# Kernel tuning notes

Hardware: AMD Instinct MI355X
Metric: run time of the kernel (lower is better)

## Reference

```python
import jax, jax.numpy as jnp
import numpy as np

D = 128      # internal_dimensions
L = 4        # num_edge_convs
N = 100000   # nodes
E = 800000   # edges
G = 64       # graphs
IN = 4       # in_channels


def _ln(x, g, b):
    m = jnp.mean(x, -1, keepdims=True)
    v = jnp.mean((x - m) ** 2, -1, keepdims=True)
    return (x - m) * jax.lax.rsqrt(v + 1e-5) * g + b


def _gelu(x):
    return jax.nn.gelu(x, approximate=False)  # torch nn.GELU default (erf)


def _seg_mean(x, seg, n):
    s = jax.ops.segment_sum(x, seg, num_segments=n)
    c = jax.ops.segment_sum(jnp.ones((x.shape[0], 1), x.dtype), seg, num_segments=n)
    return s / jnp.maximum(c, 1.0)


def _seg_max(x, seg, n):
    m = jax.ops.segment_max(x, seg, num_segments=n)
    return jnp.where(jnp.isfinite(m), m, 0.0)  # empty segments -> 0 (PyG convention)


def _forward(x, edge_index, batch, num_graphs,
             in_W1, in_b1, in_g1, in_bn1, in_W2, in_b2, in_g2, in_bn2,
             pre_g, pre_b, cW1, cb1, cg1, cbb1, cW2, cb2, cg2, cbb2, pW, pb,
             ag_g, ag_b,
             kW1, kb1, kg1, kbb1, kW2, kb2, kg2, kbb2,
             kW3, kb3, kg3, kbb3, kW4, kb4):
    n = x.shape[0]
    # input_net: Linear -> LN -> GELU -> Linear -> LN   (dropout=0, eval)
    h = _gelu(_ln(x @ in_W1 + in_b1, in_g1, in_bn1))
    h = _ln(h @ in_W2 + in_b2, in_g2, in_bn2)

    x_in_max = _seg_max(h, batch, num_graphs)
    x_in_mean = _seg_mean(h, batch, num_graphs)

    src, dst = edge_index[0], edge_index[1]  # PyG: message from src (x_j) to dst (x_i)
    xcur = h
    for l in range(L):
        identity = xcur
        hn = _ln(xcur, pre_g[l], pre_b[l])
        xi = hn[dst]            # [E, D]
        xj = hn[src]            # [E, D]
        m = jnp.concatenate([xi, xj - xi], axis=-1)       # [E, 2D]
        m = _gelu(_ln(m @ cW1[l] + cb1[l], cg1[l], cbb1[l]))
        m = _gelu(_ln(m @ cW2[l] + cb2[l], cg2[l], cbb2[l]))
        a_max = _seg_max(m, dst, n)
        a_mean = _seg_mean(m, dst, n)
        aggr = jnp.concatenate([a_max, a_mean], axis=-1)  # [N, 2D]
        xcur = identity + aggr @ pW[l] + pb[l]

    xcur = _ln(xcur, ag_g, ag_b)
    x_g_max = _seg_max(xcur, batch, num_graphs)
    x_g_mean = _seg_mean(xcur, batch, num_graphs)

    xp = jnp.concatenate([x_in_max, x_in_mean, x_g_max, x_g_mean], axis=-1)  # [G, 4D]
    z = _gelu(_ln(xp @ kW1 + kb1, kg1, kbb1))
    z = _gelu(_ln(z @ kW2 + kb2, kg2, kbb2))
    z = _gelu(_ln(z @ kW3 + kb3, kg3, kbb3))
    return z @ kW4 + kb4  # [G, 1]


def setup_inputs() -> dict:
    key = jax.random.key(0)
    ks = iter(jax.random.split(key, 64))
    def W(shape, fan):
        return jax.random.normal(next(ks), shape, jnp.float32) * np.float32((2.0 / fan) ** 0.5)
    inp = {}
    inp["x"] = jax.random.normal(next(ks), (N, IN), jnp.float32)
    inp["edge_index"] = jax.random.randint(next(ks), (2, E), 0, N)
    inp["batch"] = jnp.sort(jax.random.randint(next(ks), (N,), 0, G))
    inp["num_graphs"] = G
    inp["in_W1"] = W((IN, D), IN); inp["in_b1"] = jnp.zeros((D,), jnp.float32)
    inp["in_g1"] = jnp.ones((D,), jnp.float32); inp["in_bn1"] = jnp.zeros((D,), jnp.float32)
    inp["in_W2"] = W((D, D), D); inp["in_b2"] = jnp.zeros((D,), jnp.float32)
    inp["in_g2"] = jnp.ones((D,), jnp.float32); inp["in_bn2"] = jnp.zeros((D,), jnp.float32)
    inp["pre_g"] = jnp.ones((L, D), jnp.float32); inp["pre_b"] = jnp.zeros((L, D), jnp.float32)
    inp["cW1"] = W((L, 2 * D, D), 2 * D); inp["cb1"] = jnp.zeros((L, D), jnp.float32)
    inp["cg1"] = jnp.ones((L, D), jnp.float32); inp["cbb1"] = jnp.zeros((L, D), jnp.float32)
    inp["cW2"] = W((L, D, D), D); inp["cb2"] = jnp.zeros((L, D), jnp.float32)
    inp["cg2"] = jnp.ones((L, D), jnp.float32); inp["cbb2"] = jnp.zeros((L, D), jnp.float32)
    inp["pW"] = W((L, 2 * D, D), 2 * D); inp["pb"] = jnp.zeros((L, D), jnp.float32)
    inp["ag_g"] = jnp.ones((D,), jnp.float32); inp["ag_b"] = jnp.zeros((D,), jnp.float32)
    inp["kW1"] = W((4 * D, D), 4 * D); inp["kb1"] = jnp.zeros((D,), jnp.float32)
    inp["kg1"] = jnp.ones((D,), jnp.float32); inp["kbb1"] = jnp.zeros((D,), jnp.float32)
    inp["kW2"] = W((D, D), D); inp["kb2"] = jnp.zeros((D,), jnp.float32)
    inp["kg2"] = jnp.ones((D,), jnp.float32); inp["kbb2"] = jnp.zeros((D,), jnp.float32)
    inp["kW3"] = W((D, D // 4), D); inp["kb3"] = jnp.zeros((D // 4,), jnp.float32)
    inp["kg3"] = jnp.ones((D // 4,), jnp.float32); inp["kbb3"] = jnp.zeros((D // 4,), jnp.float32)
    inp["kW4"] = W((D // 4, 1), D // 4); inp["kb4"] = jnp.zeros((1,), jnp.float32)
    return inp


def reference(x, edge_index, batch, num_graphs,
              in_W1, in_b1, in_g1, in_bn1, in_W2, in_b2, in_g2, in_bn2,
              pre_g, pre_b, cW1, cb1, cg1, cbb1, cW2, cb2, cg2, cbb2, pW, pb,
              ag_g, ag_b,
              kW1, kb1, kg1, kbb1, kW2, kb2, kg2, kbb2,
              kW3, kb3, kg3, kbb3, kW4, kb4):
    return _forward(x, edge_index, batch, num_graphs,
                    in_W1, in_b1, in_g1, in_bn1, in_W2, in_b2, in_g2, in_bn2,
                    pre_g, pre_b, cW1, cb1, cg1, cbb1, cW2, cb2, cg2, cbb2, pW, pb,
                    ag_g, ag_b,
                    kW1, kb1, kg1, kbb1, kW2, kb2, kg2, kbb2,
                    kW3, kb3, kg3, kbb3, kW4, kb4)
```

## Files before the change

kernel.cpp:

```cpp
#include <hip/hip_runtime.h>
#include <hip/hip_bf16.h>
#include <math.h>

__device__ __forceinline__ float geluf(float x) {
    return 0.5f * x * (1.0f + erff(x * 0.70710678118654752f));
}
#define MAPNEGINF 0x007FFFFFu
__device__ __forceinline__ float funmap(unsigned m) {
    return __uint_as_float((m & 0x80000000u) ? (m ^ 0x80000000u) : ~m);
}
__device__ __forceinline__ unsigned fmap(float f) {
    unsigned u = __float_as_uint(f);
    return ((int)u < 0) ? ~u : (u | 0x80000000u);
}
__device__ __forceinline__ float wred64(float v) {
#pragma unroll
    for (int m = 1; m < 64; m <<= 1) v += __shfl_xor(v, m);
    return v;
}
__device__ __forceinline__ unsigned short bf16r(float f) {
    unsigned u = __float_as_uint(f);
    u += 0x7fffu + ((u >> 16) & 1u);
    return (unsigned short)(u >> 16);
}

__device__ __forceinline__ void stage_wq(float* Ws, const float* __restrict__ src, int t) {
#pragma unroll
    for (int it = 0; it < 4; ++it) {
        const int idx = it * 1024 + (t << 2);
        *(float4*)(Ws + idx) = *(const float4*)(src + idx);
    }
}

__device__ __forceinline__ void kloop_q(const float* As, const float* Ws, float (&acc)[4][8],
                                        const int r0, const int ogc, const int kb) {
#pragma unroll
    for (int kk = 0; kk < 32; kk += 4) {
        const float4 a0 = *(const float4*)(As + (r0 + 0) * 132 + kb + kk);
        const float4 a1 = *(const float4*)(As + (r0 + 1) * 132 + kb + kk);
        const float4 a2 = *(const float4*)(As + (r0 + 2) * 132 + kb + kk);
        const float4 a3 = *(const float4*)(As + (r0 + 3) * 132 + kb + kk);
#define MAD8(R, AV)                                                                     \
    {                                                                                   \
        acc[R][0] += (AV)*wA.x; acc[R][1] += (AV)*wA.y; acc[R][2] += (AV)*wA.z;         \
        acc[R][3] += (AV)*wA.w; acc[R][4] += (AV)*wB.x; acc[R][5] += (AV)*wB.y;         \
        acc[R][6] += (AV)*wB.z; acc[R][7] += (AV)*wB.w;                                 \
    }
#define KSTEP(J, C)                                                                     \
    {                                                                                   \
        const float4 wA = *(const float4*)(Ws + (kk + (J)) * 128 + ogc);                \
        const float4 wB = *(const float4*)(Ws + (kk + (J)) * 128 + 64 + ogc);           \
        MAD8(0, a0.C) MAD8(1, a1.C) MAD8(2, a2.C) MAD8(3, a3.C)                         \
    }
        KSTEP(0, x) KSTEP(1, y) KSTEP(2, z) KSTEP(3, w)
#undef KSTEP
#undef MAD8
    }
}

__global__ void k_zero(unsigned* __restrict__ p, int n) {
    const int i = blockIdx.x * 256 + threadIdx.x;
    if (i < n) p[i] = 0u;
}

__global__ void k_copyu(const unsigned* __restrict__ a, const unsigned* __restrict__ b,
                        unsigned* __restrict__ ac, unsigned* __restrict__ bc, int n) {
    const int i = blockIdx.x * 256 + threadIdx.x;
    if (i < n) {
        ac[i] = a[i];
        bc[i] = b[i];
    }
}

__global__ void k_count(const int* __restrict__ ei, unsigned* __restrict__ deg, int E) {
    const int e = blockIdx.x * 256 + threadIdx.x;
    if (e < E) atomicAdd(deg + ei[E + e], 1u);
}

__global__ void k_scan1(const unsigned* __restrict__ deg, unsigned* __restrict__ excl,
                        unsigned* __restrict__ bsum, int n) {
    __shared__ unsigned sh[256];
    const int t = threadIdx.x;
    const int base = blockIdx.x * 1024 + t * 4;
    unsigned v0 = (base + 0 < n) ? deg[base + 0] : 0u;
    unsigned v1 = (base + 1 < n) ? deg[base + 1] : 0u;
    unsigned v2 = (base + 2 < n) ? deg[base + 2] : 0u;
    unsigned v3 = (base + 3 < n) ? deg[base + 3] : 0u;
    const unsigned s = v0 + v1 + v2 + v3;
    sh[t] = s;
    __syncthreads();
    for (int off = 1; off < 256; off <<= 1) {
        unsigned x = 0;
        if (t >= off) x = sh[t - off];
        __syncthreads();
        if (t >= off) sh[t] += x;
        __syncthreads();
    }
    const unsigned ebase = sh[t] - s;
    if (base + 0 < n) excl[base + 0] = ebase;
    if (base + 1 < n) excl[base + 1] = ebase + v0;
    if (base + 2 < n) excl[base + 2] = ebase + v0 + v1;
    if (base + 3 < n) excl[base + 3] = ebase + v0 + v1 + v2;
    if (t == 255) bsum[blockIdx.x] = sh[255];
}

__global__ void k_scan2(unsigned* __restrict__ bsum, int nb) {
    __shared__ unsigned sh[256];
    const int t = threadIdx.x;
    const unsigned v = (t < nb) ? bsum[t] : 0u;
    sh[t] = v;
    __syncthreads();
    for (int off = 1; off < 256; off <<= 1) {
        unsigned x = 0;
        if (t >= off) x = sh[t - off];
        __syncthreads();
        if (t >= off) sh[t] += x;
        __syncthreads();
    }
    if (t < nb) bsum[t] = sh[t] - v;
}

__global__ void k_scan3(unsigned* __restrict__ excl, const unsigned* __restrict__ bsum, int n) {
    const int t = threadIdx.x;
    const int base = blockIdx.x * 1024 + t * 4;
    const unsigned add = bsum[blockIdx.x];
#pragma unroll
    for (int j = 0; j < 4; ++j)
        if (base + j < n) excl[base + j] += add;
}

__global__ void k_scatter(const int* __restrict__ ei, unsigned* __restrict__ cursor,
                          int* __restrict__ esrc, int* __restrict__ edst, int E) {
    const int e = blockIdx.x * 256 + threadIdx.x;
    if (e < E) {
        const int s = ei[e];
        const int d = ei[E + e];
        const unsigned pos = atomicAdd(cursor + d, 1u);
        esrc[pos] = s;
        edst[pos] = d;
    }
}

__global__ void k_in1(const float* __restrict__ x, const float* __restrict__ W1,
                      const float* __restrict__ b1, const float* __restrict__ g1,
                      const float* __restrict__ bn1, float* __restrict__ h, int n) {
    const int t = threadIdx.x, lane = t & 63, wave = t >> 6;
    const int d0 = lane << 1;
    const float2 w0 = *(const float2*)(W1 + d0);
    const float2 w1 = *(const float2*)(W1 + 128 + d0);
    const float2 w2 = *(const float2*)(W1 + 256 + d0);
    const float2 w3 = *(const float2*)(W1 + 384 + d0);
    const float2 bb = *(const float2*)(b1 + d0);
    const float2 gg = *(const float2*)(g1 + d0);
    const float2 nn = *(const float2*)(bn1 + d0);
    const int stride = gridDim.x * 4;
    for (int node = blockIdx.x * 4 + wave; node < n; node += stride) {
        const float4 xv = *(const float4*)(x + (size_t)node * 4);
        float h0 = bb.x + xv.x * w0.x + xv.y * w1.x + xv.z * w2.x + xv.w * w3.x;
        float h1 = bb.y + xv.x * w0.y + xv.y * w1.y + xv.z * w2.y + xv.w * w3.y;
        const float s = wred64(h0 + h1), q = wred64(h0 * h0 + h1 * h1);
        const float mean = s * 0.0078125f, var = q * 0.0078125f - mean * mean;
        const float rs = rsqrtf(var + 1e-5f);
        h0 = geluf((h0 - mean) * rs * gg.x + nn.x);
        h1 = geluf((h1 - mean) * rs * gg.y + nn.y);
        *(float2*)(h + (size_t)node * 128 + d0) = make_float2(h0, h1);
    }
}

__global__ __launch_bounds__(256, 2) void k_in2(const float* __restrict__ A,
                                                const float* __restrict__ W,
                                                const float* __restrict__ bias,
                                                const float* __restrict__ g,
                                                const float* __restrict__ b,
                                                float* __restrict__ C, int n) {
    __shared__ float As[64 * 132];
    __shared__ float Ws[4096];
    const int t = threadIdx.x;
    const int n0 = blockIdx.x * 64;
    {
        const int r = t >> 2, c0 = (t & 3) << 5;
        const int row = n0 + r;
        const bool ok = row < n;
#pragma unroll
        for (int j = 0; j < 8; ++j) {
            const int col = c0 + (j << 2);
            float4 v = make_float4(0.f, 0.f, 0.f, 0.f);
            if (ok) v = *(const float4*)(A + (size_t)row * 128 + col);
            *(float4*)(As + r * 132 + col) = v;
        }
    }
    float acc[4][8];
#pragma unroll
    for (int r = 0; r < 4; ++r)
#pragma unroll
        for (int o = 0; o < 8; ++o) acc[r][o] = 0.f;
    const int og = t & 15, eg = t >> 4;
    const int ogc = og << 2, r0 = eg << 2;
#pragma unroll
    for (int q4 = 0; q4 < 4; ++q4) {
        stage_wq(Ws, W + q4 * 4096, t);
        __syncthreads();
        kloop_q(As, Ws, acc, r0, ogc, q4 * 32);
        __syncthreads();
    }
    const float4 bA = *(const float4*)(bias + ogc);
    const float4 bB = *(const float4*)(bias + 64 + ogc);
    const float4 gA = *(const float4*)(g + ogc);
    const float4 gB = *(const float4*)(g + 64 + ogc);
    const float4 lA = *(const float4*)(b + ogc);
    const float4 lB = *(const float4*)(b + 64 + ogc);
#pragma unroll
    for (int r = 0; r < 4; ++r) {
        float v[8];
        v[0] = acc[r][0] + bA.x; v[1] = acc[r][1] + bA.y;
        v[2] = acc[r][2] + bA.z; v[3] = acc[r][3] + bA.w;
        v[4] = acc[r][4] + bB.x; v[5] = acc[r][5] + bB.y;
        v[6] = acc[r][6] + bB.z; v[7] = acc[r][7] + bB.w;
        float s = 0.f, q = 0.f;
#pragma unroll
        for (int o = 0; o < 8; ++o) { s += v[o]; q += v[o] * v[o]; }
#pragma unroll
        for (int m = 1; m < 16; m <<= 1) { s += __shfl_xor(s, m); q += __shfl_xor(q, m); }
        const float mean = s * 0.0078125f;
        const float var = q * 0.0078125f - mean * mean;
        const float rs = rsqrtf(var + 1e-5f);
        const int row = n0 + r0 + r;
        if (row < n) {
            *(float4*)(C + (size_t)row * 128 + ogc) = make_float4(
                (v[0] - mean) * rs * gA.x + lA.x, (v[1] - mean) * rs * gA.y + lA.y,
                (v[2] - mean) * rs * gA.z + lA.z, (v[3] - mean) * rs * gA.w + lA.w);
            *(float4*)(C + (size_t)row * 128 + 64 + ogc) = make_float4(
                (v[4] - mean) * rs * gB.x + lB.x, (v[5] - mean) * rs * gB.y + lB.y,
                (v[6] - mean) * rs * gB.z + lB.z, (v[7] - mean) * rs * gB.w + lB.w);
        }
    }
}

__global__ void k_ln(const float* __restrict__ in, const float* __restrict__ g,
                     const float* __restrict__ b, float* __restrict__ out, int n) {
    const int t = threadIdx.x, lane = t & 63, wave = t >> 6;
    const int d0 = lane << 1;
    const float ga = g[d0], gb = g[d0 + 1], ba = b[d0], bb = b[d0 + 1];
    const int stride = gridDim.x * 4;
    for (int node = blockIdx.x * 4 + wave; node < n; node += stride) {
        const float2 v = *(const float2*)(in + (size_t)node * 128 + d0);
        const float s = wred64(v.x + v.y), q = wred64(v.x * v.x + v.y * v.y);
        const float mean = s * 0.0078125f, var = q * 0.0078125f - mean * mean;
        const float rs = rsqrtf(var + 1e-5f);
        *(float2*)(out + (size_t)node * 128 + d0) =
            make_float2((v.x - mean) * rs * ga + ba, (v.y - mean) * rs * gb + bb);
    }
}

__global__ void k_wxj(const float* __restrict__ c, float* __restrict__ Wx,
                      float* __restrict__ Wj) {
    const int idx = blockIdx.x * 256 + threadIdx.x;
    const float a = c[idx], b = c[16384 + idx];
    Wx[idx] = a - b;
    Wj[idx] = b;
}

__global__ __launch_bounds__(256, 2) void k_gemmh(const float* __restrict__ A,
                                                  const float* __restrict__ W,
                                                  const float* __restrict__ bias,
                                                  unsigned short* __restrict__ C, int n) {
    __shared__ float As[64 * 132];
    __shared__ float Ws[4096];
    const int t = threadIdx.x;
    const int n0 = blockIdx.x * 64;
    {
        const int r = t >> 2, c0 = (t & 3) << 5;
        const int row = n0 + r;
        const bool ok = row < n;
#pragma unroll
        for (int j = 0; j < 8; ++j) {
            const int col = c0 + (j << 2);
            float4 v = make_float4(0.f, 0.f, 0.f, 0.f);
            if (ok) v = *(const float4*)(A + (size_t)row * 128 + col);
            *(float4*)(As + r * 132 + col) = v;
        }
    }
    float acc[4][8];
#pragma unroll
    for (int r = 0; r < 4; ++r)
#pragma unroll
        for (int o = 0; o < 8; ++o) acc[r][o] = 0.f;
    const int og = t & 15, eg = t >> 4;
    const int ogc = og << 2, r0 = eg << 2;
#pragma unroll
    for (int q4 = 0; q4 < 4; ++q4) {
        stage_wq(Ws, W + q4 * 4096, t);
        __syncthreads();
        kloop_q(As, Ws, acc, r0, ogc, q4 * 32);
        __syncthreads();
    }
    float4 bA = make_float4(0.f, 0.f, 0.f, 0.f), bB = bA;
    if (bias) {
        bA = *(const float4*)(bias + ogc);
        bB = *(const float4*)(bias + 64 + ogc);
    }
#pragma unroll
    for (int r = 0; r < 4; ++r) {
        const int row = n0 + r0 + r;
        if (row < n) {
            ushort4 u0, u1;
            u0.x = bf16r(acc[r][0] + bA.x); u0.y = bf16r(acc[r][1] + bA.y);
            u0.z = bf16r(acc[r][2] + bA.z); u0.w = bf16r(acc[r][3] + bA.w);
            u1.x = bf16r(acc[r][4] + bB.x); u1.y = bf16r(acc[r][5] + bB.y);
            u1.z = bf16r(acc[r][6] + bB.z); u1.w = bf16r(acc[r][7] + bB.w);
            *(ushort4*)(C + (size_t)row * 128 + ogc) = u0;
            *(ushort4*)(C + (size_t)row * 128 + 64 + ogc) = u1;
        }
    }
}

__global__ __launch_bounds__(256, 2) void k_edge(
    const unsigned short* __restrict__ P, const unsigned short* __restrict__ Q,
    const int* __restrict__ esrc, const int* __restrict__ edst, const float* __restrict__ W2,
    const float* __restrict__ g1, const float* __restrict__ b1, const float* __restrict__ cb2,
    const float* __restrict__ g2, const float* __restrict__ b2,
    const unsigned* __restrict__ rowend, const unsigned* __restrict__ degc,
    float* __restrict__ amax, float* __restrict__ asum, float* __restrict__ recmax,
    float* __restrict__ recsum, int* __restrict__ recid, int E) {
    __shared__ float Us[64 * 132];
    __shared__ float Ws[4096];
    __shared__ int sdst[64], ssrc[64], sdg[64];
    __shared__ float scb2[128], sg2[128], sb2[128];
    const int t = threadIdx.x;
    const int base = blockIdx.x * 512;
    if (t >= 128) {
        const int d = t - 128;
        scb2[d] = cb2[d];
        sg2[d] = g2[d];
        sb2[d] = b2[d];
    }
    const int lane = t & 63, wave = t >> 6;
    const int d0 = lane << 1;
    const float g1a = g1[d0], g1b = g1[d0 + 1], b1a = b1[d0], b1b = b1[d0 + 1];
    const int og = t & 15, eg = t >> 4;
    const int ogc = og << 2, r0 = eg << 2;
    int cur = -1, istart = 0;
    float vmax = -INFINITY, vsum = 0.f;
    int id0 = -1, id1 = -1;

    for (int s8 = 0; s8 < 8; ++s8) {
        const int sb = base + s8 * 64;
        __syncthreads();
        if (t < 64) {
            const int idx = sb + t;
            const int ci = idx < E ? idx : (E - 1);
            ssrc[t] = esrc[ci];
            const int d = edst[ci];
            sdg[t] = d;
            sdst[t] = (idx < E) ? d : -1;
        }
        __syncthreads();
#pragma unroll 4
        for (int p = 0; p < 16; ++p) {
            const int i = (p << 2) + wave;
            const unsigned pu = *(const unsigned*)(P + ((size_t)sdg[i] << 7) + d0);
            const unsigned qu = *(const unsigned*)(Q + ((size_t)ssrc[i] << 7) + d0);
            const float x0 = __uint_as_float(pu << 16) + __uint_as_float(qu << 16);
            const float x1 =
                __uint_as_float(pu & 0xffff0000u) + __uint_as_float(qu & 0xffff0000u);
            const float s = wred64(x0 + x1);
            const float q = wred64(x0 * x0 + x1 * x1);
            const float mean = s * 0.0078125f;
            const float var = q * 0.0078125f - mean * mean;
            const float rs = rsqrtf(var + 1e-5f);
            const float y0 = geluf((x0 - mean) * rs * g1a + b1a);
            const float y1 = geluf((x1 - mean) * rs * g1b + b1b);
            *(float2*)(Us + i * 132 + d0) = make_float2(y0, y1);
        }
        float acc[4][8];
#pragma unroll
        for (int r = 0; r < 4; ++r)
#pragma unroll
            for (int o = 0; o < 8; ++o) acc[r][o] = 0.f;
#pragma unroll
        for (int q4 = 0; q4 < 4; ++q4) {
            stage_wq(Ws, W2 + q4 * 4096, t);
            __syncthreads();
            kloop_q(Us, Ws, acc, r0, ogc, q4 * 32);
            __syncthreads();
        }
#pragma unroll
        for (int r = 0; r < 4; ++r) {
            float v[8];
            float s = 0.f, q = 0.f;
#pragma unroll
            for (int o = 0; o < 8; ++o) {
                const int col = (o < 4) ? (ogc + o) : (64 + ogc + o - 4);
                v[o] = acc[r][o] + scb2[col];
                s += v[o];
                q += v[o] * v[o];
            }
#pragma unroll
            for (int m = 1; m < 16; m <<= 1) { s += __shfl_xor(s, m); q += __shfl_xor(q, m); }
            const float mean = s * 0.0078125f;
            const float var = q * 0.0078125f - mean * mean;
            const float rs = rsqrtf(var + 1e-5f);
#pragma unroll
            for (int o = 0; o < 8; ++o) {
                const int col = (o < 4) ? (ogc + o) : (64 + ogc + o - 4);
                v[o] = geluf((v[o] - mean) * rs * sg2[col] + sb2[col]);
            }
            *(float4*)(Us + (r0 + r) * 132 + ogc) = make_float4(v[0], v[1], v[2], v[3]);
            *(float4*)(Us + (r0 + r) * 132 + 64 + ogc) = make_float4(v[4], v[5], v[6], v[7]);
        }
        __syncthreads();
        if (t < 128) {
            for (int i = 0; i < 64; ++i) {
                const int dn = sdst[i];
                const int gi = s8 * 64 + i;
                if (dn != cur) {
                    if (cur >= 0) {
                        const unsigned re = rowend[cur];
                        const unsigned rs0 = re - degc[cur];
                        const unsigned ps = (unsigned)(base + istart);
                        const unsigned pe = (unsigned)(base + gi);
                        if (ps == rs0 && pe == re) {
                            amax[(size_t)cur * 128 + t] = vmax;
                            asum[(size_t)cur * 128 + t] = vsum;
                        } else {
                            const int slot = (istart == 0) ? 0 : 1;
                            const size_t ro = (size_t)(2 * blockIdx.x + slot) * 128 + t;
                            recmax[ro] = vmax;
                            recsum[ro] = vsum;
                            if (slot == 0) id0 = cur; else id1 = cur;
                        }
                    }
                    cur = dn;
                    istart = gi;
                    vmax = -INFINITY;
                    vsum = 0.f;
                }
                if (dn >= 0) {
                    const float v = Us[i * 132 + t];
                    vmax = fmaxf(vmax, v);
                    vsum += v;
                }
            }
        }
    }
    if (t < 128 && cur >= 0) {
        const int iend = min(512, E - base);
        const unsigned re = rowend[cur];
        const unsigned rs0 = re - degc[cur];
        const unsigned ps = (unsigned)(base + istart);
        const unsigned pe = (unsigned)(base + iend);
        if (ps == rs0 && pe == re) {
            amax[(size_t)cur * 128 + t] = vmax;
            asum[(size_t)cur * 128 + t] = vsum;
        } else {
            const int slot = (istart == 0) ? 0 : 1;
            const size_t ro = (size_t)(2 * blockIdx.x + slot) * 128 + t;
            recmax[ro] = vmax;
            recsum[ro] = vsum;
            if (slot == 0) id0 = cur; else id1 = cur;
        }
    }
    if (t == 0) {
        recid[2 * blockIdx.x] = id0;
        recid[2 * blockIdx.x + 1] = id1;
    }
}

__global__ void k_merge(const unsigned* __restrict__ rowend, const unsigned* __restrict__ degc,
                        const float* __restrict__ recmax, const float* __restrict__ recsum,
                        const int* __restrict__ recid, float* __restrict__ amax,
                        float* __restrict__ asum, int n) {
    const int node = blockIdx.x * 2 + (threadIdx.x >> 7);
    const int t = threadIdx.x & 127;
    if (node >= n) return;
    const unsigned dg = degc[node];
    if (dg == 0u) {
        amax[(size_t)node * 128 + t] = 0.f;
        asum[(size_t)node * 128 + t] = 0.f;
        return;
    }
    const unsigned re = rowend[node], rs = re - dg;
    const int b0 = rs >> 9, b1 = (re - 1) >> 9;
    if (b0 == b1) return;
    float m = -INFINITY, s = 0.f;
    for (int b = b0; b <= b1; ++b) {
#pragma unroll
        for (int sl = 0; sl < 2; ++sl) {
            if (recid[2 * b + sl] == node) {
                const size_t ro = (size_t)(2 * b + sl) * 128 + t;
                m = fmaxf(m, recmax[ro]);
                s += recsum[ro];
            }
        }
    }
    amax[(size_t)node * 128 + t] = m;
    asum[(size_t)node * 128 + t] = s;
}

__global__ __launch_bounds__(256, 2) void k_update(const float* __restrict__ amax,
                                                   const float* __restrict__ asum,
                                                   const unsigned* __restrict__ degc,
                                                   const float* __restrict__ pW,
                                                   const float* __restrict__ pb,
                                                   float* __restrict__ xcur, int n) {
    __shared__ float As[64 * 132];
    __shared__ float Ws[4096];
    const int t = threadIdx.x;
    const int n0 = blockIdx.x * 64;
    const int og = t & 15, eg = t >> 4;
    const int ogc = og << 2, r0 = eg << 2;
    float acc[4][8];
#pragma unroll
    for (int r = 0; r < 4; ++r)
#pragma unroll
        for (int o = 0; o < 8; ++o) acc[r][o] = 0.f;
    const int r = t >> 2, c0 = (t & 3) << 5;
    const int row = n0 + r;
    const bool ok = row < n;
#pragma unroll
    for (int pass = 0; pass < 2; ++pass) {
        if (pass == 0) {
#pragma unroll
            for (int j = 0; j < 8; ++j) {
                const int col = c0 + (j << 2);
                float4 v = make_float4(0.f, 0.f, 0.f, 0.f);
                if (ok) v = *(const float4*)(amax + (size_t)row * 128 + col);
                *(float4*)(As + r * 132 + col) = v;
            }
        } else {
            float inv = 0.f;
            if (ok) {
                const unsigned dv = degc[row];
                inv = 1.f / (float)(dv < 1u ? 1u : dv);
            }
#pragma unroll
            for (int j = 0; j < 8; ++j) {
                const int col = c0 + (j << 2);
                float4 v = make_float4(0.f, 0.f, 0.f, 0.f);
                if (ok) {
                    const float4 sv = *(const float4*)(asum + (size_t)row * 128 + col);
                    v = make_float4(sv.x * inv, sv.y * inv, sv.z * inv, sv.w * inv);
                }
                *(float4*)(As + r * 132 + col) = v;
            }
        }
#pragma unroll
        for (int q4 = 0; q4 < 4; ++q4) {
            stage_wq(Ws, pW + (size_t)(pass * 128 + q4 * 32) * 128, t);
            __syncthreads();
            kloop_q(As, Ws, acc, r0, ogc, q4 * 32);
            __syncthreads();
        }
    }
    const float4 bA = *(const float4*)(pb + ogc);
    const float4 bB = *(const float4*)(pb + 64 + ogc);
#pragma unroll
    for (int rr = 0; rr < 4; ++rr) {
        const int orow = n0 + r0 + rr;
        if (orow < n) {
            const float4 x0 = *(const float4*)(xcur + (size_t)orow * 128 + ogc);
            const float4 x1 = *(const float4*)(xcur + (size_t)orow * 128 + 64 + ogc);
            *(float4*)(xcur + (size_t)orow * 128 + ogc) =
                make_float4(x0.x + acc[rr][0] + bA.x, x0.y + acc[rr][1] + bA.y,
                            x0.z + acc[rr][2] + bA.z, x0.w + acc[rr][3] + bA.w);
            *(float4*)(xcur + (size_t)orow * 128 + 64 + ogc) =
                make_float4(x1.x + acc[rr][4] + bB.x, x1.y + acc[rr][5] + bB.y,
                            x1.z + acc[rr][6] + bB.z, x1.w + acc[rr][7] + bB.w);
        }
    }
}

__global__ void k_pool_init(unsigned* __restrict__ gmax1, float* __restrict__ gsum1,
                            unsigned* __restrict__ gcount1, unsigned* __restrict__ gmax2,
                            float* __restrict__ gsum2, unsigned* __restrict__ gcount2, int ng) {
    const int i = blockIdx.x * 256 + threadIdx.x;
    if (i < ng * 128) {
        gmax1[i] = MAPNEGINF;
        gsum1[i] = 0.f;
        gmax2[i] = MAPNEGINF;
        gsum2[i] = 0.f;
    }
    if (i < ng) {
        gcount1[i] = 0u;
        gcount2[i] = 0u;
    }
}

__global__ void k_pool(const float* __restrict__ in, const int* __restrict__ batch,
                       unsigned* __restrict__ gmax, float* __restrict__ gsum,
                       unsigned* __restrict__ gcount, int n) {
    const int t = threadIdx.x;
    if (t >= 128) return;
    const int per = (n + gridDim.x - 1) / gridDim.x;
    const int i0 = blockIdx.x * per;
    const int i1 = min(n, i0 + per);
    if (i0 >= i1) return;
    int cur = batch[i0];
    float vmax = -INFINITY, vsum = 0.f;
    unsigned cnt = 0;
    for (int i = i0; i < i1; ++i) {
        const int g = batch[i];
        if (g != cur) {
            atomicMax(gmax + (size_t)cur * 128 + t, fmap(vmax));
            atomicAdd(gsum + (size_t)cur * 128 + t, vsum);
            if (t == 0) atomicAdd(gcount + cur, cnt);
            cur = g;
            vmax = -INFINITY;
            vsum = 0.f;
            cnt = 0;
        }
        const float v = in[(size_t)i * 128 + t];
        vmax = fmaxf(vmax, v);
        vsum += v;
        cnt++;
    }
    atomicMax(gmax + (size_t)cur * 128 + t, fmap(vmax));
    atomicAdd(gsum + (size_t)cur * 128 + t, vsum);
    if (t == 0) atomicAdd(gcount + cur, cnt);
}

__global__ void k_xp(const unsigned* __restrict__ gmax1, const float* __restrict__ gsum1,
                     const unsigned* __restrict__ gcount1, const unsigned* __restrict__ gmax2,
                     const float* __restrict__ gsum2, const unsigned* __restrict__ gcount2,
                     float* __restrict__ xp) {
    const int g = blockIdx.x, d = threadIdx.x;
    const unsigned c1u = gcount1[g], c2u = gcount2[g];
    const float c1 = (float)(c1u < 1u ? 1u : c1u);
    const float c2 = (float)(c2u < 1u ? 1u : c2u);
    const unsigned m1 = gmax1[g * 128 + d], m2 = gmax2[g * 128 + d];
    xp[g * 512 + d] = (m1 == MAPNEGINF) ? 0.f : funmap(m1);
    xp[g * 512 + 128 + d] = gsum1[g * 128 + d] / c1;
    xp[g * 512 + 256 + d] = (m2 == MAPNEGINF) ? 0.f : funmap(m2);
    xp[g * 512 + 384 + d] = gsum2[g * 128 + d] / c2;
}

__global__ __launch_bounds__(64) void k_know(
    const float* __restrict__ xp, const float* __restrict__ kW1, const float* __restrict__ kb1,
    const float* __restrict__ kg1, const float* __restrict__ kbb1, const float* __restrict__ kW2,
    const float* __restrict__ kb2, const float* __restrict__ kg2, const float* __restrict__ kbb2,
    const float* __restrict__ kW3, const float* __restrict__ kb3, const float* __restrict__ kg3,
    const float* __restrict__ kbb3, const float* __restrict__ kW4, const float* __restrict__ kb4,
    float* __restrict__ out) {
    __shared__ float sh[512];
    __shared__ float s3[32];
    const int l = threadIdx.x, g = blockIdx.x;
    const int d0 = l << 1;
    *(float4*)(sh + l * 8) = *(const float4*)(xp + g * 512 + l * 8);
    *(float4*)(sh + l * 8 + 4) = *(const float4*)(xp + g * 512 + l * 8 + 4);
    __syncthreads();
    float a0 = kb1[d0], a1 = kb1[d0 + 1];
    for (int k = 0; k < 512; ++k) {
        const float u = sh[k];
        const float2 w = *(const float2*)(kW1 + k * 128 + d0);
        a0 += u * w.x;
        a1 += u * w.y;
    }
    {
        const float s = wred64(a0 + a1), q = wred64(a0 * a0 + a1 * a1);
        const float mean = s * 0.0078125f, var = q * 0.0078125f - mean * mean;
        const float rs = rsqrtf(var + 1e-5f);
        a0 = geluf((a0 - mean) * rs * kg1[d0] + kbb1[d0]);
        a1 = geluf((a1 - mean) * rs * kg1[d0 + 1] + kbb1[d0 + 1]);
    }
    __syncthreads();
    sh[d0] = a0;
    sh[d0 + 1] = a1;
    __syncthreads();
    float b0v = kb2[d0], b1v = kb2[d0 + 1];
    for (int k = 0; k < 128; ++k) {
        const float u = sh[k];
        const float2 w = *(const float2*)(kW2 + k * 128 + d0);
        b0v += u * w.x;
        b1v += u * w.y;
    }
    {
        const float s = wred64(b0v + b1v), q = wred64(b0v * b0v + b1v * b1v);
        const float mean = s * 0.0078125f, var = q * 0.0078125f - mean * mean;
        const float rs = rsqrtf(var + 1e-5f);
        b0v = geluf((b0v - mean) * rs * kg2[d0] + kbb2[d0]);
        b1v = geluf((b1v - mean) * rs * kg2[d0 + 1] + kbb2[d0 + 1]);
    }
    __syncthreads();
    sh[d0] = b0v;
    sh[d0 + 1] = b1v;
    __syncthreads();
    const int d3 = (l & 15) << 1;
    float c0 = kb3[d3], c1 = kb3[d3 + 1];
    for (int k = 0; k < 128; ++k) {
        const float u = sh[k];
        const float2 w = *(const float2*)(kW3 + k * 32 + d3);
        c0 += u * w.x;
        c1 += u * w.y;
    }
    {
        float s = c0 + c1, q = c0 * c0 + c1 * c1;
#pragma unroll
        for (int m = 1; m < 16; m <<= 1) {
            s += __shfl_xor(s, m);
            q += __shfl_xor(q, m);
        }
        const float mean = s * 0.03125f, var = q * 0.03125f - mean * mean;
        const float rs = rsqrtf(var + 1e-5f);
        c0 = geluf((c0 - mean) * rs * kg3[d3] + kbb3[d3]);
        c1 = geluf((c1 - mean) * rs * kg3[d3 + 1] + kbb3[d3 + 1]);
    }
    if (l < 16) {
        s3[d3] = c0;
        s3[d3 + 1] = c1;
    }
    __syncthreads();
    if (l == 0) {
        float rr = kb4[0];
        for (int k = 0; k < 32; ++k) rr += s3[k] * kW4[k];
        out[g] = rr;
    }
}

extern "C" void kernel_launch(void* const* d_in, const int* in_sizes, int n_in, void* d_out,
                              int out_size, void* d_ws, size_t ws_size, hipStream_t stream) {
    const int N = in_sizes[0] / 4;
    const int E = in_sizes[1] / 2;
    const int G = 64;
    const int L = 4;

    const float* x = (const float*)d_in[0];
    const int* ei = (const int*)d_in[1];
    const int* batch = (const int*)d_in[2];
    const float* inW1 = (const float*)d_in[4];
    const float* inb1 = (const float*)d_in[5];
    const float* ing1 = (const float*)d_in[6];
    const float* inbn1 = (const float*)d_in[7];
    const float* inW2 = (const float*)d_in[8];
    const float* inb2 = (const float*)d_in[9];
    const float* ing2 = (const float*)d_in[10];
    const float* inbn2 = (const float*)d_in[11];
    const float* pre_g = (const float*)d_in[12];
    const float* pre_b = (const float*)d_in[13];
    const float* cW1 = (const float*)d_in[14];
    const float* cb1 = (const float*)d_in[15];
    const float* cg1 = (const float*)d_in[16];
    const float* cbb1 = (const float*)d_in[17];
    const float* cW2 = (const float*)d_in[18];
    const float* cb2 = (const float*)d_in[19];
    const float* cg2 = (const float*)d_in[20];
    const float* cbb2 = (const float*)d_in[21];
    const float* pW = (const float*)d_in[22];
    const float* pb = (const float*)d_in[23];
    const float* ag_g = (const float*)d_in[24];
    const float* ag_b = (const float*)d_in[25];
    const float* kW1 = (const float*)d_in[26];
    const float* kb1 = (const float*)d_in[27];
    const float* kg1 = (const float*)d_in[28];
    const float* kbb1 = (const float*)d_in[29];
    const float* kW2 = (const float*)d_in[30];
    const float* kb2 = (const float*)d_in[31];
    const float* kg2 = (const float*)d_in[32];
    const float* kbb2 = (const float*)d_in[33];
    const float* kW3 = (const float*)d_in[34];
    const float* kb3 = (const float*)d_in[35];
    const float* kg3 = (const float*)d_in[36];
    const float* kbb3 = (const float*)d_in[37];
    const float* kW4 = (const float*)d_in[38];
    const float* kb4 = (const float*)d_in[39];
    float* out = (float*)d_out;

    const int nblkE = (E + 511) / 512;

    char* wsb = (char*)d_ws;
    size_t off = 0;
    auto ALC = [&](size_t bytes) {
        void* p = wsb + off;
        off = (off + bytes + 255) & ~(size_t)255;
        return p;
    };
    const size_t NB = (size_t)N * 128 * 4;
    float* xcur = (float*)ALC(NB);
    float* hn = (float*)ALC(NB);
    float* amax = hn;
    float* asum = (float*)ALC(NB);
    unsigned short* Pb = (unsigned short*)ALC((size_t)N * 128 * 2);
    unsigned short* Qb = (unsigned short*)ALC((size_t)N * 128 * 2);
    unsigned* deg = (unsigned*)ALC((size_t)N * 4);
    unsigned* cursor = (unsigned*)ALC((size_t)N * 4);
    unsigned* degc = (unsigned*)ALC((size_t)N * 4);
    unsigned* rowend = (unsigned*)ALC((size_t)N * 4);
    unsigned* bsum = (unsigned*)ALC(4096);
    int* esrc = (int*)ALC((size_t)E * 4);
    int* edst = (int*)ALC((size_t)E * 4);
    float* recmax = (float*)ALC((size_t)nblkE * 2 * 128 * 4);
    float* recsum = (float*)ALC((size_t)nblkE * 2 * 128 * 4);
    int* recid = (int*)ALC((size_t)nblkE * 2 * 4);
    float* Wx = (float*)ALC(65536);
    float* Wj = (float*)ALC(65536);
    unsigned* gmax1 = (unsigned*)ALC((size_t)G * 128 * 4);
    float* gsum1 = (float*)ALC((size_t)G * 128 * 4);
    unsigned* gcount1 = (unsigned*)ALC((size_t)G * 4);
    unsigned* gmax2 = (unsigned*)ALC((size_t)G * 128 * 4);
    float* gsum2 = (float*)ALC((size_t)G * 128 * 4);
    unsigned* gcount2 = (unsigned*)ALC((size_t)G * 4);
    float* xp = (float*)ALC((size_t)G * 512 * 4);

    if (off > ws_size) {
        k_zero<<<(out_size + 255) / 256, 256, 0, stream>>>((unsigned*)d_out, out_size);
        return;
    }

    k_zero<<<(N + 255) / 256, 256, 0, stream>>>(deg, N);
    k_count<<<(E + 255) / 256, 256, 0, stream>>>(ei, deg, E);
    const int nb = (N + 1023) / 1024;
    k_scan1<<<nb, 256, 0, stream>>>(deg, cursor, bsum, N);
    k_scan2<<<1, 256, 0, stream>>>(bsum, nb);
    k_scan3<<<nb, 256, 0, stream>>>(cursor, bsum, N);
    k_scatter<<<(E + 255) / 256, 256, 0, stream>>>(ei, cursor, esrc, edst, E);
    k_copyu<<<(N + 255) / 256, 256, 0, stream>>>(deg, cursor, degc, rowend, N);

    const int gemmGrid = (N + 63) / 64;
    k_in1<<<1024, 256, 0, stream>>>(x, inW1, inb1, ing1, inbn1, hn, N);
    k_in2<<<gemmGrid, 256, 0, stream>>>(hn, inW2, inb2, ing2, inbn2, xcur, N);
    k_pool_init<<<(G * 128 + 255) / 256, 256, 0, stream>>>(gmax1, gsum1, gcount1, gmax2, gsum2,
                                                           gcount2, G);
    k_pool<<<512, 256, 0, stream>>>(xcur, batch, gmax1, gsum1, gcount1, N);

    for (int l = 0; l < L; ++l) {
        k_wxj<<<64, 256, 0, stream>>>(cW1 + (size_t)l * 32768, Wx, Wj);
        k_ln<<<1024, 256, 0, stream>>>(xcur, pre_g + l * 128, pre_b + l * 128, hn, N);
        k_gemmh<<<gemmGrid, 256, 0, stream>>>(hn, Wx, cb1 + l * 128, Pb, N);
        k_gemmh<<<gemmGrid, 256, 0, stream>>>(hn, Wj, (const float*)nullptr, Qb, N);
        k_edge<<<nblkE, 256, 0, stream>>>(Pb, Qb, esrc, edst, cW2 + (size_t)l * 16384,
                                          cg1 + l * 128, cbb1 + l * 128, cb2 + l * 128,
                                          cg2 + l * 128, cbb2 + l * 128, rowend, degc, amax, asum,
                                          recmax, recsum, recid, E);
        k_merge<<<(N + 1) / 2, 256, 0, stream>>>(rowend, degc, recmax, recsum, recid, amax, asum,
                                                 N);
        k_update<<<gemmGrid, 256, 0, stream>>>(amax, asum, degc, pW + (size_t)l * 32768,
                                               pb + l * 128, xcur, N);
    }

    k_ln<<<1024, 256, 0, stream>>>(xcur, ag_g, ag_b, hn, N);
    k_pool<<<512, 256, 0, stream>>>(hn, batch, gmax2, gsum2, gcount2, N);
    k_xp<<<G, 128, 0, stream>>>(gmax1, gsum1, gcount1, gmax2, gsum2, gcount2, xp);
    k_know<<<G, 64, 0, stream>>>(xp, kW1, kb1, kg1, kbb1, kW2, kb2, kg2, kbb2, kW3, kb3, kg3,
                                 kbb3, kW4, kb4, out);
}
```

Measured before the change: 95.78 ms.

## Split edge kernel into chunked gather pass and per-64-edge GEMM pass

The fused edge kernel (gather + LN/GELU + GEMM + segmented aggregation over 512 edges per block) is split into two kernels. A grid-stride gather kernel writes the normalized first-layer activations to an fp32 chunk buffer, and a GEMM kernel handles 64 edges per block with the segment reduction. Edges are processed in chunks so the buffer can stay cache-resident, and the merge and record granularity moves from 512 to 64 edges. The mean division also moves into a separate k_mean kernel. In exchange the activations make an extra round trip through memory, and there are more launches, more partial records to merge, and more weight restaging per block.

```diff
diff --git a/kernel.cpp b/kernel.cpp
--- a/kernel.cpp
+++ b/kernel.cpp
@@ -314,155 +314,144 @@
     }
 }
 
-__global__ __launch_bounds__(256, 2) void k_edge(
-    const unsigned short* __restrict__ P, const unsigned short* __restrict__ Q,
-    const int* __restrict__ esrc, const int* __restrict__ edst, const float* __restrict__ W2,
-    const float* __restrict__ g1, const float* __restrict__ b1, const float* __restrict__ cb2,
-    const float* __restrict__ g2, const float* __restrict__ b2,
+__global__ void k_gather(const unsigned short* __restrict__ P,
+                         const unsigned short* __restrict__ Q, const int* __restrict__ esrc,
+                         const int* __restrict__ edst, const float* __restrict__ g1,
+                         const float* __restrict__ b1, float* __restrict__ U, int e0, int e1) {
+    const int t = threadIdx.x, lane = t & 63, wave = t >> 6;
+    const int d0 = lane << 1;
+    const float ga = g1[d0], gb = g1[d0 + 1], ba = b1[d0], bb = b1[d0 + 1];
+    const int stride = gridDim.x * 4;
+    for (int e = e0 + blockIdx.x * 4 + wave; e < e1; e += stride) {
+        const int s = esrc[e], d = edst[e];
+        const unsigned pu = *(const unsigned*)(P + ((size_t)d << 7) + d0);
+        const unsigned qu = *(const unsigned*)(Q + ((size_t)s << 7) + d0);
+        const float x0 = __uint_as_float(pu << 16) + __uint_as_float(qu << 16);
+        const float x1 = __uint_as_float(pu & 0xffff0000u) + __uint_as_float(qu & 0xffff0000u);
+        const float su = wred64(x0 + x1);
+        const float qq = wred64(x0 * x0 + x1 * x1);
+        const float mean = su * 0.0078125f;
+        const float var = qq * 0.0078125f - mean * mean;
+        const float rs = rsqrtf(var + 1e-5f);
+        *(float2*)(U + (size_t)(e - e0) * 128 + d0) = make_float2(
+            geluf((x0 - mean) * rs * ga + ba), geluf((x1 - mean) * rs * gb + bb));
+    }
+}
+
+__global__ __launch_bounds__(256, 2) void k_gemme(
+    const float* __restrict__ U, const int* __restrict__ edst, const float* __restrict__ W2,
+    const float* __restrict__ cb2, const float* __restrict__ g2, const float* __restrict__ b2,
     const unsigned* __restrict__ rowend, const unsigned* __restrict__ degc,
     float* __restrict__ amax, float* __restrict__ asum, float* __restrict__ recmax,
-    float* __restrict__ recsum, int* __restrict__ recid, int E) {
+    float* __restrict__ recsum, int* __restrict__ recid, int e0, int E) {
     __shared__ float Us[64 * 132];
     __shared__ float Ws[4096];
-    __shared__ int sdst[64], ssrc[64], sdg[64];
+    __shared__ int sdst[64];
     __shared__ float scb2[128], sg2[128], sb2[128];
     const int t = threadIdx.x;
-    const int base = blockIdx.x * 512;
+    const int base = e0 + blockIdx.x * 64;
+    if (base >= E) return;
+    const int gb = base >> 6;
+    if (t < 64) {
+        const int idx = base + t;
+        sdst[t] = (idx < E) ? edst[idx] : -1;
+    }
     if (t >= 128) {
         const int d = t - 128;
         scb2[d] = cb2[d];
         sg2[d] = g2[d];
         sb2[d] = b2[d];
     }
-    const int lane = t & 63, wave = t >> 6;
-    const int d0 = lane << 1;
-    const float g1a = g1[d0], g1b = g1[d0 + 1], b1a = b1[d0], b1b = b1[d0 + 1];
+    {
+        const int r = t >> 2, c0 = (t & 3) << 5;
+        const bool ok = (base + r) < E;
+        const float* src = U + (size_t)(base - e0 + r) * 128;
+#pragma unroll
+        for (int j = 0; j < 8; ++j) {
+            const int col = c0 + (j << 2);
+            float4 v = make_float4(0.f, 0.f, 0.f, 0.f);
+            if (ok) v = *(const float4*)(src + col);
+            *(float4*)(Us + r * 132 + col) = v;
+        }
+    }
+    float acc[4][8];
+#pragma unroll
+    for (int r = 0; r < 4; ++r)
+#pragma unroll
+        for (int o = 0; o < 8; ++o) acc[r][o] = 0.f;
     const int og = t & 15, eg = t >> 4;
     const int ogc = og << 2, r0 = eg << 2;
-    int cur = -1, istart = 0;
-    float vmax = -INFINITY, vsum = 0.f;
-    int id0 = -1, id1 = -1;
-
-    for (int s8 = 0; s8 < 8; ++s8) {
-        const int sb = base + s8 * 64;
-        __syncthreads();
-        if (t < 64) {
-            const int idx = sb + t;
-            const int ci = idx < E ? idx : (E - 1);
-            ssrc[t] = esrc[ci];
-            const int d = edst[ci];
-            sdg[t] = d;
-            sdst[t] = (idx < E) ? d : -1;
-        }
-        __syncthreads();
-#pragma unroll 4
-        for (int p = 0; p < 16; ++p) {
-            const int i = (p << 2) + wave;
-            const unsigned pu = *(const unsigned*)(P + ((size_t)sdg[i] << 7) + d0);
-            const unsigned qu = *(const unsigned*)(Q + ((size_t)ssrc[i] << 7) + d0);
-            const float x0 = __uint_as_float(pu << 16) + __uint_as_float(qu << 16);
-            const float x1 =
-                __uint_as_float(pu & 0xffff0000u) + __uint_as_float(qu & 0xffff0000u);
-            const float s = wred64(x0 + x1);
-            const float q = wred64(x0 * x0 + x1 * x1);
-            const float mean = s * 0.0078125f;
-            const float var = q * 0.0078125f - mean * mean;
-            const float rs = rsqrtf(var + 1e-5f);
-            const float y0 = geluf((x0 - mean) * rs * g1a + b1a);
-            const float y1 = geluf((x1 - mean) * rs * g1b + b1b);
-            *(float2*)(Us + i * 132 + d0) = make_float2(y0, y1);
-        }
-        float acc[4][8];
-#pragma unroll
-        for (int r = 0; r < 4; ++r)
-#pragma unroll
-            for (int o = 0; o < 8; ++o) acc[r][o] = 0.f;
-#pragma unroll
-        for (int q4 = 0; q4 < 4; ++q4) {
-            stage_wq(Ws, W2 + q4 * 4096, t);
-            __syncthreads();
-            kloop_q(Us, Ws, acc, r0, ogc, q4 * 32);
-            __syncthreads();
-        }
-#pragma unroll
-        for (int r = 0; r < 4; ++r) {
-            float v[8];
-            float s = 0.f, q = 0.f;
-#pragma unroll
-            for (int o = 0; o < 8; ++o) {
-                const int col = (o < 4) ? (ogc + o) : (64 + ogc + o - 4);
-                v[o] = acc[r][o] + scb2[col];
-                s += v[o];
-                q += v[o] * v[o];
+#pragma unroll
+    for (int q4 = 0; q4 < 4; ++q4) {
+        stage_wq(Ws, W2 + q4 * 4096, t);
+        __syncthreads();
+        kloop_q(Us, Ws, acc, r0, ogc, q4 * 32);
+        __syncthreads();
+    }
+#pragma unroll
+    for (int r = 0; r < 4; ++r) {
+        float v[8];
+        float s = 0.f, q = 0.f;
+#pragma unroll
+        for (int o = 0; o < 8; ++o) {
+            const int col = (o < 4) ? (ogc + o) : (64 + ogc + o - 4);
+            v[o] = acc[r][o] + scb2[col];
+            s += v[o];
+            q += v[o] * v[o];
+        }
+#pragma unroll
+        for (int m = 1; m < 16; m <<= 1) { s += __shfl_xor(s, m); q += __shfl_xor(q, m); }
+        const float mean = s * 0.0078125f;
+        const float var = q * 0.0078125f - mean * mean;
+        const float rs = rsqrtf(var + 1e-5f);
+#pragma unroll
+        for (int o = 0; o < 8; ++o) {
+            const int col = (o < 4) ? (ogc + o) : (64 + ogc + o - 4);
+            v[o] = geluf((v[o] - mean) * rs * sg2[col] + sb2[col]);
+        }
+        *(float4*)(Us + (r0 + r) * 132 + ogc) = make_float4(v[0], v[1], v[2], v[3]);
+        *(float4*)(Us + (r0 + r) * 132 + 64 + ogc) = make_float4(v[4], v[5], v[6], v[7]);
+    }
+    __syncthreads();
+    if (t < 128) {
+        int cur = sdst[0], istart = 0;
+        float vmax = -INFINITY, vsum = 0.f;
+        int id0 = -1, id1 = -1;
+        auto flush = [&](int iend) {
+            const unsigned re = rowend[cur];
+            const unsigned rs0 = re - degc[cur];
+            const unsigned ps = (unsigned)(base + istart), pe = (unsigned)(base + iend);
+            if (ps == rs0 && pe == re) {
+                amax[(size_t)cur * 128 + t] = vmax;
+                asum[(size_t)cur * 128 + t] = vsum;
+            } else {
+                const int slot = (istart == 0) ? 0 : 1;
+                const size_t ro = (size_t)(2 * gb + slot) * 128 + t;
+                recmax[ro] = vmax;
+                recsum[ro] = vsum;
+                if (slot == 0) id0 = cur; else id1 = cur;
             }
-#pragma unroll
-            for (int m = 1; m < 16; m <<= 1) { s += __shfl_xor(s, m); q += __shfl_xor(q, m); }
-            const float mean = s * 0.0078125f;
-            const float var = q * 0.0078125f - mean * mean;
-            const float rs = rsqrtf(var + 1e-5f);
-#pragma unroll
-            for (int o = 0; o < 8; ++o) {
-                const int col = (o < 4) ? (ogc + o) : (64 + ogc + o - 4);
-                v[o] = geluf((v[o] - mean) * rs * sg2[col] + sb2[col]);
+        };
+        for (int i = 0; i < 64; ++i) {
+            const int dn = sdst[i];
+            if (dn != cur) {
+                if (cur >= 0) flush(i);
+                cur = dn;
+                istart = i;
+                vmax = -INFINITY;
+                vsum = 0.f;
             }
-            *(float4*)(Us + (r0 + r) * 132 + ogc) = make_float4(v[0], v[1], v[2], v[3]);
-            *(float4*)(Us + (r0 + r) * 132 + 64 + ogc) = make_float4(v[4], v[5], v[6], v[7]);
-        }
-        __syncthreads();
-        if (t < 128) {
-            for (int i = 0; i < 64; ++i) {
-                const int dn = sdst[i];
-                const int gi = s8 * 64 + i;
-                if (dn != cur) {
-                    if (cur >= 0) {
-                        const unsigned re = rowend[cur];
-                        const unsigned rs0 = re - degc[cur];
-                        const unsigned ps = (unsigned)(base + istart);
-                        const unsigned pe = (unsigned)(base + gi);
-                        if (ps == rs0 && pe == re) {
-                            amax[(size_t)cur * 128 + t] = vmax;
-                            asum[(size_t)cur * 128 + t] = vsum;
-                        } else {
-                            const int slot = (istart == 0) ? 0 : 1;
-                            const size_t ro = (size_t)(2 * blockIdx.x + slot) * 128 + t;
-                            recmax[ro] = vmax;
-                            recsum[ro] = vsum;
-                            if (slot == 0) id0 = cur; else id1 = cur;
-                        }
-                    }
-                    cur = dn;
-                    istart = gi;
-                    vmax = -INFINITY;
-                    vsum = 0.f;
-                }
-                if (dn >= 0) {
-                    const float v = Us[i * 132 + t];
-                    vmax = fmaxf(vmax, v);
-                    vsum += v;
-                }
+            if (dn >= 0) {
+                const float v = Us[i * 132 + t];
+                vmax = fmaxf(vmax, v);
+                vsum += v;
             }
         }
-    }
-    if (t < 128 && cur >= 0) {
-        const int iend = min(512, E - base);
-        const unsigned re = rowend[cur];
-        const unsigned rs0 = re - degc[cur];
-        const unsigned ps = (unsigned)(base + istart);
-        const unsigned pe = (unsigned)(base + iend);
-        if (ps == rs0 && pe == re) {
-            amax[(size_t)cur * 128 + t] = vmax;
-            asum[(size_t)cur * 128 + t] = vsum;
-        } else {
-            const int slot = (istart == 0) ? 0 : 1;
-            const size_t ro = (size_t)(2 * blockIdx.x + slot) * 128 + t;
-            recmax[ro] = vmax;
-            recsum[ro] = vsum;
-            if (slot == 0) id0 = cur; else id1 = cur;
-        }
-    }
-    if (t == 0) {
-        recid[2 * blockIdx.x] = id0;
-        recid[2 * blockIdx.x + 1] = id1;
+        if (cur >= 0) flush(64);
+        if (t == 0) {
+            recid[2 * gb] = id0;
+            recid[2 * gb + 1] = id1;
+        }
     }
 }
 
@@ -480,7 +469,7 @@
         return;
     }
     const unsigned re = rowend[node], rs = re - dg;
-    const int b0 = rs >> 9, b1 = (re - 1) >> 9;
+    const int b0 = rs >> 6, b1 = (re - 1) >> 6;
     if (b0 == b1) return;
     float m = -INFINITY, s = 0.f;
     for (int b = b0; b <= b1; ++b) {
@@ -497,9 +486,18 @@
     asum[(size_t)node * 128 + t] = s;
 }
 
+__global__ void k_mean(float* __restrict__ asum, const unsigned* __restrict__ degc, int n32) {
+    for (int i = blockIdx.x * 256 + threadIdx.x; i < n32; i += gridDim.x * 256) {
+        const int row = i >> 5;
+        const unsigned dv = degc[row];
+        const float inv = 1.f / (float)(dv < 1u ? 1u : dv);
+        float4 v = ((float4*)asum)[i];
+        ((float4*)asum)[i] = make_float4(v.x * inv, v.y * inv, v.z * inv, v.w * inv);
+    }
+}
+
 __global__ __launch_bounds__(256, 2) void k_update(const float* __restrict__ amax,
-                                                   const float* __restrict__ asum,
-                                                   const unsigned* __restrict__ degc,
+                                                   const float* __restrict__ amean,
                                                    const float* __restrict__ pW,
                                                    const float* __restrict__ pb,
                                                    float* __restrict__ xcur, int n) {
@@ -519,30 +517,13 @@
     const bool ok = row < n;
 #pragma unroll
     for (int pass = 0; pass < 2; ++pass) {
-        if (pass == 0) {
-#pragma unroll
-            for (int j = 0; j < 8; ++j) {
-                const int col = c0 + (j << 2);
-                float4 v = make_float4(0.f, 0.f, 0.f, 0.f);
-                if (ok) v = *(const float4*)(amax + (size_t)row * 128 + col);
-                *(float4*)(As + r * 132 + col) = v;
-            }
-        } else {
-            float inv = 0.f;
-            if (ok) {
-                const unsigned dv = degc[row];
-                inv = 1.f / (float)(dv < 1u ? 1u : dv);
-            }
-#pragma unroll
-            for (int j = 0; j < 8; ++j) {
-                const int col = c0 + (j << 2);
-                float4 v = make_float4(0.f, 0.f, 0.f, 0.f);
-                if (ok) {
-                    const float4 sv = *(const float4*)(asum + (size_t)row * 128 + col);
-                    v = make_float4(sv.x * inv, sv.y * inv, sv.z * inv, sv.w * inv);
-                }
-                *(float4*)(As + r * 132 + col) = v;
-            }
+        const float* src = (pass == 0) ? amax : amean;
+#pragma unroll
+        for (int j = 0; j < 8; ++j) {
+            const int col = c0 + (j << 2);
+            float4 v = make_float4(0.f, 0.f, 0.f, 0.f);
+            if (ok) v = *(const float4*)(src + (size_t)row * 128 + col);
+            *(float4*)(As + r * 132 + col) = v;
         }
 #pragma unroll
         for (int q4 = 0; q4 < 4; ++q4) {
@@ -764,7 +745,10 @@
     const float* kb4 = (const float*)d_in[39];
     float* out = (float*)d_out;
 
-    const int nblkE = (E + 511) / 512;
+    const int CHUNK_BLOCKS = 782;
+    const int CHUNK_E = CHUNK_BLOCKS * 64;
+    const int nblk64 = (E + 63) / 64;
+    const int nchunks = (nblk64 + CHUNK_BLOCKS - 1) / CHUNK_BLOCKS;
 
     char* wsb = (char*)d_ws;
     size_t off = 0;
@@ -780,6 +764,7 @@
     float* asum = (float*)ALC(NB);
     unsigned short* Pb = (unsigned short*)ALC((size_t)N * 128 * 2);
     unsigned short* Qb = (unsigned short*)ALC((size_t)N * 128 * 2);
+    float* U = (float*)ALC((size_t)CHUNK_E * 128 * 4);
     unsigned* deg = (unsigned*)ALC((size_t)N * 4);
     unsigned* cursor = (unsigned*)ALC((size_t)N * 4);
     unsigned* degc = (unsigned*)ALC((size_t)N * 4);
@@ -787,9 +772,9 @@
     unsigned* bsum = (unsigned*)ALC(4096);
     int* esrc = (int*)ALC((size_t)E * 4);
     int* edst = (int*)ALC((size_t)E * 4);
-    float* recmax = (float*)ALC((size_t)nblkE * 2 * 128 * 4);
-    float* recsum = (float*)ALC((size_t)nblkE * 2 * 128 * 4);
-    int* recid = (int*)ALC((size_t)nblkE * 2 * 4);
+    float* recmax = (float*)ALC((size_t)nblk64 * 2 * 128 * 4);
+    float* recsum = (float*)ALC((size_t)nblk64 * 2 * 128 * 4);
+    int* recid = (int*)ALC((size_t)nblk64 * 2 * 4);
     float* Wx = (float*)ALC(65536);
     float* Wj = (float*)ALC(65536);
     unsigned* gmax1 = (unsigned*)ALC((size_t)G * 128 * 4);
@@ -826,14 +811,21 @@
         k_ln<<<1024, 256, 0, stream>>>(xcur, pre_g + l * 128, pre_b + l * 128, hn, N);
         k_gemmh<<<gemmGrid, 256, 0, stream>>>(hn, Wx, cb1 + l * 128, Pb, N);
         k_gemmh<<<gemmGrid, 256, 0, stream>>>(hn, Wj, (const float*)nullptr, Qb, N);
-        k_edge<<<nblkE, 256, 0, stream>>>(Pb, Qb, esrc, edst, cW2 + (size_t)l * 16384,
-                                          cg1 + l * 128, cbb1 + l * 128, cb2 + l * 128,
-                                          cg2 + l * 128, cbb2 + l * 128, rowend, degc, amax, asum,
-                                          recmax, recsum, recid, E);
+        for (int c = 0; c < nchunks; ++c) {
+            const int e0 = c * CHUNK_E;
+            const int e1 = min(E, e0 + CHUNK_E);
+            if (e0 >= E) break;
+            k_gather<<<2048, 256, 0, stream>>>(Pb, Qb, esrc, edst, cg1 + l * 128, cbb1 + l * 128,
+                                               U, e0, e1);
+            k_gemme<<<CHUNK_BLOCKS, 256, 0, stream>>>(
+                U, edst, cW2 + (size_t)l * 16384, cb2 + l * 128, cg2 + l * 128, cbb2 + l * 128,
+                rowend, degc, amax, asum, recmax, recsum, recid, e0, E);
+        }
         k_merge<<<(N + 1) / 2, 256, 0, stream>>>(rowend, degc, recmax, recsum, recid, amax, asum,
                                                  N);
-        k_update<<<gemmGrid, 256, 0, stream>>>(amax, asum, degc, pW + (size_t)l * 32768,
-                                               pb + l * 128, xcur, N);
+        k_mean<<<2048, 256, 0, stream>>>(asum, degc, N * 32);
+        k_update<<<gemmGrid, 256, 0, stream>>>(amax, asum, pW + (size_t)l * 32768, pb + l * 128,
+                                               xcur, N);
     }
 
     k_ln<<<1024, 256, 0, stream>>>(xcur, ag_g, ag_b, hn, N);
```

New measurement: 97.47 ms. About the same (+1.8%).
